# Performance work log

Measured on AMD Instinct MI355X. Metric: run time of the kernel, lower is better.

## Reference

```python
import jax, jax.numpy as jnp
import numpy as np

B, S, D, H = 32, 512, 640, 10
DK = D // H           # 64
NUM_ITER = 3          # capsule routing iterations


def _proj(x, W, b):
    # [B,S,D] @ [D,D]^T -> split heads -> [B,H,S,DK]
    b_, s_, _ = x.shape
    return (x @ W.T + b).reshape(b_, s_, H, DK).transpose(0, 2, 1, 3)


def _squash(t, eps=1e-9):
    sn = jnp.sum(t * t, axis=-1, keepdims=True)
    return (sn / (1.0 + sn)) * t / jnp.sqrt(sn + eps)


def setup_inputs() -> dict:
    key0 = jax.random.key(0)
    ks = jax.random.split(key0, 12)
    s = 1.0 / np.sqrt(D)
    return {
        "query": jax.random.normal(ks[0], (B, S, D), jnp.float32),
        "key": jax.random.normal(ks[1], (B, S, D), jnp.float32),
        "value": jax.random.normal(ks[2], (B, S, D), jnp.float32),
        "mask": jax.random.randint(ks[3], (B, 1, S, S), 0, 2, jnp.int32),
        "adj": jax.random.uniform(ks[4], (B, S, S), jnp.float32),
        "layer": 2,
        "Wq": jax.random.normal(ks[5], (D, D), jnp.float32) * s,
        "bq": jnp.zeros((D,), jnp.float32),
        "Wk": jax.random.normal(ks[6], (D, D), jnp.float32) * s,
        "bk": jnp.zeros((D,), jnp.float32),
        "Wv": jax.random.normal(ks[7], (D, D), jnp.float32) * s,
        "bv": jnp.zeros((D,), jnp.float32),
        # capsule route weights: [num_capsules=1, num_route_nodes=H, DK, D]
        "route_weights": jax.random.normal(ks[8], (1, H, DK, D), jnp.float32) * 0.05,
    }


def reference(query, key, value, mask, adj, layer,
              Wq, bq, Wk, bk, Wv, bv, route_weights):
    q = _proj(query, Wq, bq)   # [B,H,S,DK]
    k = _proj(key, Wk, bk)
    v = _proj(value, Wv, bv)

    # scaled dot-product scores, adjacency + layer-dependent modulation
    scores = jnp.einsum('bhqd,bhkd->bhqk', q, k) / jnp.sqrt(jnp.float32(DK))
    scores = scores + adj[:, None, :, :] / jnp.float32(layer + 1)
    scores = jnp.where(mask == 0, jnp.float32(-1e9), scores)
    p_attn = jax.nn.softmax(scores, axis=-1)            # [B,H,S,S]
    x = jnp.einsum('bhqk,bhkd->bhqd', p_attn, v)        # [B,H,S,DK]

    # [B,H,S,DK] -> [B*S, H, DK]: per-token capsule routing over heads
    x = x.transpose(0, 2, 1, 3).reshape(B * S, H, DK)

    # priors: [num_caps=1, N, H(route nodes), D]
    priors = jnp.einsum('nri,crio->cnro', x, route_weights)
    logits = jnp.zeros(priors.shape[:-1] + (1,), priors.dtype)  # [1,N,H,1]
    out = None
    for i in range(NUM_ITER):
        probs = jax.nn.softmax(logits, axis=2)                  # over route nodes
        out = _squash(jnp.sum(probs * priors, axis=2, keepdims=True))  # [1,N,1,D]
        if i != NUM_ITER - 1:
            logits = logits + jnp.sum(priors * out, axis=-1, keepdims=True)

    return out.reshape(B, S, D)
```

## Files before the change

### kernel.cpp

```cpp
#include <hip/hip_runtime.h>
#include <stdint.h>

#define BB 32
#define SS 512
#define DD 640
#define HH 10
#define DKK 64
#define NTOK (BB*SS)

using f32x4  = __attribute__((ext_vector_type(4))) float;
using bf16x8 = __attribute__((ext_vector_type(8))) __bf16;
using u32x4  = __attribute__((ext_vector_type(4))) unsigned int;
using u32x2  = __attribute__((ext_vector_type(2))) unsigned int;
using u16x4  = __attribute__((ext_vector_type(4))) unsigned short;
using i32x4  = __attribute__((ext_vector_type(4))) int;

__device__ inline unsigned short f2bf(float f){
  union { float f; unsigned int u; } v; v.f=f;
  unsigned int u=v.u;
  u += 0x7FFFu + ((u>>16)&1u);
  return (unsigned short)(u>>16);
}
__device__ inline float bf2f(unsigned short s){
  union { unsigned int u; float f; } v; v.u = ((unsigned int)s)<<16;
  return v.f;
}
__device__ inline unsigned int cvtpk_bf16(float lo, float hi){
  unsigned int r;
  asm volatile("v_cvt_pk_bf16_f32 %0, %1, %2" : "=v"(r) : "v"(lo), "v"(hi));
  return r;
}
__device__ inline void gload_lds16(const unsigned short* g, unsigned short* l){
  __builtin_amdgcn_global_load_lds(
      (const __attribute__((address_space(1))) unsigned int*)g,
      (__attribute__((address_space(3))) unsigned int*)l, 16, 0, 0);
}

__global__ void convert_qkv(const float* __restrict__ q, const float* __restrict__ k,
                            const float* __restrict__ v,
                            unsigned short* __restrict__ xq, unsigned short* __restrict__ xk,
                            unsigned short* __restrict__ xv){
  int i = blockIdx.x*blockDim.x + threadIdx.x;
  const int n4 = (NTOK*DD)/4;
  for (; i < n4; i += gridDim.x*blockDim.x){
    f32x4 a = ((const f32x4*)q)[i];
    f32x4 b = ((const f32x4*)k)[i];
    f32x4 c = ((const f32x4*)v)[i];
    u16x4 ra, rb, rc;
    #pragma unroll
    for (int j=0;j<4;j++){ ra[j]=f2bf(a[j]); rb[j]=f2bf(b[j]); rc[j]=f2bf(c[j]); }
    ((u16x4*)xq)[i]=ra; ((u16x4*)xk)[i]=rb; ((u16x4*)xv)[i]=rc;
  }
}

__global__ void convert_w(const float* __restrict__ wq, const float* __restrict__ wk,
                          const float* __restrict__ wv, const float* __restrict__ rw,
                          unsigned short* __restrict__ bwq, unsigned short* __restrict__ bwk,
                          unsigned short* __restrict__ bwv, unsigned short* __restrict__ brwt){
  int i = blockIdx.x*blockDim.x + threadIdx.x;
  if (i < DD*DD){
    bwq[i]=f2bf(wq[i]); bwk[i]=f2bf(wk[i]); bwv[i]=f2bf(wv[i]);
    unsigned short r = f2bf(rw[i]);
    int ri = i / DD, o = i % DD;
    brwt[o*DD + ri] = r;
  }
}

__global__ void bias_kernel(const int* __restrict__ mask, const float* __restrict__ adj,
                            const int* __restrict__ layer, unsigned short* __restrict__ biasT){
  float sc = 1.0f/(float)(layer[0]+1);
  int i = blockIdx.x*blockDim.x + threadIdx.x;
  const int n4 = (BB*SS*SS)/4;
  for (; i < n4; i += gridDim.x*blockDim.x){
    i32x4 m = ((const i32x4*)mask)[i];
    f32x4 a = ((const f32x4*)adj)[i];
    u16x4 r;
    #pragma unroll
    for (int j=0;j<4;j++) r[j] = m[j] ? f2bf(a[j]*sc) : f2bf(-1e9f);
    const int e  = i*4;
    const int bb = e >> 18;
    const int qq = (e >> 9) & 511;
    const int kk = e & 511;
    const int idx = (((bb*32 + (qq>>4))*32 + (kk>>4))<<8) + ((qq&15)<<4) + (kk&15);
    *(u16x4*)(biasT + idx) = r;
  }
}

#define BM 128
#define BN 128
#define BK 32

template<typename EPI>
__device__ inline void gemm_body(const unsigned short* __restrict__ A,
                                 const unsigned short* __restrict__ W,
                                 int m0, int n0, EPI&& epi)
{
  __shared__ unsigned short As[2][BM*BK];
  __shared__ unsigned short Ws[2][BN*BK];
  const int tid  = threadIdx.x;
  const int lane = tid & 63;
  const int wave = tid >> 6;
  const int wr   = (wave >> 1) * 64;
  const int wc   = (wave & 1) * 64;
  const int l15  = lane & 15;
  const int g    = lane >> 4;

  f32x4 acc[4][4];
  #pragma unroll
  for (int i=0;i<4;i++)
    #pragma unroll
    for (int j=0;j<4;j++){ f32x4 z = {0.f,0.f,0.f,0.f}; acc[i][j]=z; }

  const int srow  = (lane >> 2);
  const int sunit = (lane & 3) ^ ((lane >> 3) & 3);
  const unsigned short* Ag0 = A + (int64_t)(m0 + wave*32 + srow)*DD + sunit*8;
  const unsigned short* Ag1 = A + (int64_t)(m0 + wave*32 + 16 + srow)*DD + sunit*8;
  const unsigned short* Wg0 = W + (int64_t)(n0 + wave*32 + srow)*DD + sunit*8;
  const unsigned short* Wg1 = W + (int64_t)(n0 + wave*32 + 16 + srow)*DD + sunit*8;

  auto stage = [&](int buf, int k0){
    gload_lds16(Ag0 + k0, As[buf] + wave*1024);
    gload_lds16(Ag1 + k0, As[buf] + wave*1024 + 512);
    gload_lds16(Wg0 + k0, Ws[buf] + wave*1024);
    gload_lds16(Wg1 + k0, Ws[buf] + wave*1024 + 512);
  };

  const int fro = (g ^ ((l15 >> 1) & 3)) * 8;

  stage(0, 0);
  int it = 0;
  for (int k0 = 0; k0 < DD; k0 += BK, it++){
    const int buf = it & 1;
    __syncthreads();
    if (k0 + BK < DD) stage(buf^1, k0 + BK);
    bf16x8 af[4], wf[4];
    #pragma unroll
    for (int m=0;m<4;m++) af[m] = *(const bf16x8*)&As[buf][(wr + m*16 + l15)*BK + fro];
    #pragma unroll
    for (int n=0;n<4;n++) wf[n] = *(const bf16x8*)&Ws[buf][(wc + n*16 + l15)*BK + fro];
    #pragma unroll
    for (int m=0;m<4;m++)
      #pragma unroll
      for (int n=0;n<4;n++)
        acc[m][n] = __builtin_amdgcn_mfma_f32_16x16x32_bf16(af[m], wf[n], acc[m][n], 0,0,0);
  }

  #pragma unroll
  for (int m=0;m<4;m++){
    const int rowbase = m0 + wr + m*16 + g*4;
    #pragma unroll
    for (int n=0;n<4;n++){
      const int col = n0 + wc + n*16 + l15;
      #pragma unroll
      for (int r=0;r<4;r++)
        epi(rowbase + r, col, acc[m][n][r]);
    }
  }
}

__global__ __launch_bounds__(256)
void qkv_gemm(const unsigned short* __restrict__ Xq, const unsigned short* __restrict__ Xk,
              const unsigned short* __restrict__ Xv,
              const unsigned short* __restrict__ bWq, const unsigned short* __restrict__ bWk,
              const unsigned short* __restrict__ bWv,
              const float* __restrict__ bq, const float* __restrict__ bk,
              const float* __restrict__ bv,
              unsigned short* __restrict__ qbuf, unsigned short* __restrict__ kbuf,
              unsigned short* __restrict__ vTbuf)
{
  const int y   = blockIdx.y;
  const int sel = y / 5;
  const int n0  = (y % 5) * BN;
  const int m0  = blockIdx.x * BM;
  const unsigned short* A = sel==0 ? Xq  : sel==1 ? Xk  : Xv;
  const unsigned short* W = sel==0 ? bWq : sel==1 ? bWk : bWv;
  const float*          bb= sel==0 ? bq  : sel==1 ? bk  : bv;
  unsigned short* outp    = sel==0 ? qbuf : kbuf;

  gemm_body(A, W, m0, n0, [&](int row, int col, float v){
    float val = v + bb[col];
    int b=row>>9, s=row&511, h=col>>6, dk=col&63;
    if (sel < 2)
      outp[(((int64_t)(b*HH + h))*SS + s)*DKK + dk] = f2bf(val);
    else
      vTbuf[(((int64_t)(b*HH + h))*DKK + dk)*SS + s] = f2bf(val);
  });
}

__global__ __launch_bounds__(256)
void final_gemm(const unsigned short* __restrict__ A, const unsigned short* __restrict__ W,
                float* __restrict__ outp)
{
  gemm_body(A, W, blockIdx.x*BM, blockIdx.y*BN, [&](int row, int col, float v){
    outp[(int64_t)row*DD + col] = v;
  });
}

__global__ __launch_bounds__(256)
void attn_kernel(const unsigned short* __restrict__ qb, const unsigned short* __restrict__ kb,
                 const unsigned short* __restrict__ vT, const unsigned short* __restrict__ biasT,
                 unsigned short* __restrict__ xout)
{
  __shared__ unsigned short SH[20480];
  unsigned short* Kl = SH;
  unsigned short* Vl = SH + 8192;
  char* Pall = (char*)(SH + 16384);

  const int tid  = threadIdx.x;
  const int lane = tid & 63;
  const int wave = tid >> 6;
  const int l15  = lane & 15;
  const int g    = lane >> 4;

  const int orig = blockIdx.x;
  const int wgid = (orig & 7)*320 + (orig >> 3);
  const int h  = wgid % 10;
  const int qt = (wgid / 10) & 7;
  const int b  = wgid / 80;
  const int bh = b*HH + h;

  const unsigned short* Q  = qb + (int64_t)bh*SS*DKK;
  const unsigned short* K  = kb + (int64_t)bh*SS*DKK;
  const unsigned short* V  = vT + (int64_t)bh*DKK*SS;
  const unsigned short* Bt = biasT + (int64_t)((b*32 + qt*4 + wave)*32)*256
                           + l15*16 + g*4;

  const int q0 = qt*64 + wave*16;
  char* Pb = Pall + wave*2048;

  const int srow8 = lane >> 3;
  const int sunit = (lane & 7) ^ (srow8 & 7);

  bf16x8 qf[2];
  #pragma unroll
  for (int ks=0; ks<2; ks++)
    qf[ks] = *(const bf16x8*)(Q + (q0 + l15)*DKK + ks*32 + g*8);

  auto stage = [&](int c, int buf){
    #pragma unroll
    for (int c2=0;c2<2;c2++){
      const int i = wave*2 + c2;
      gload_lds16(K + (int64_t)(c*64 + i*8 + srow8)*DKK + sunit*8,
                  Kl + buf*4096 + i*512);
      gload_lds16(V + (int64_t)(i*8 + srow8)*SS + c*64 + sunit*8,
                  Vl + buf*4096 + i*512);
    }
  };

  float lsum = 0.f;
  f32x4 oacc[4];
  #pragma unroll
  for (int n=0;n<4;n++){ f32x4 z={0.f,0.f,0.f,0.f}; oacc[n]=z; }

  u16x4 bvc[4], bvn[4];
  #pragma unroll
  for (int j=0;j<4;j++) bvc[j] = *(const u16x4*)(Bt + j*256);

  stage(0, 0);
  for (int c = 0; c < 8; c++){
    const int buf = c & 1;
    __syncthreads();
    if (c < 7){
      stage(c+1, buf^1);
      #pragma unroll
      for (int j=0;j<4;j++) bvn[j] = *(const u16x4*)(Bt + ((c+1)*4 + j)*256);
    }

    f32x4 sc[4];
    #pragma unroll
    for (int j=0;j<4;j++){ f32x4 z={0.f,0.f,0.f,0.f}; sc[j]=z; }
    #pragma unroll
    for (int ks=0; ks<2; ks++){
      #pragma unroll
      for (int j=0;j<4;j++){
        bf16x8 kf = *(const bf16x8*)((char*)(Kl + buf*4096)
                     + (j*16 + l15)*128 + (((ks*4+g) ^ (l15&7))*16));
        sc[j] = __builtin_amdgcn_mfma_f32_16x16x32_bf16(kf, qf[ks], sc[j], 0,0,0);
      }
    }
    #pragma unroll
    for (int j=0;j<4;j++){
      float p[4];
      #pragma unroll
      for (int r=0;r<4;r++){
        float s = __builtin_fmaf(sc[j][r], 0.125f, bf2f(bvc[j][r]));
        p[r] = __expf(s - 8.0f);
        lsum += p[r];
      }
      unsigned int w0 = cvtpk_bf16(p[0], p[1]);
      unsigned int w1 = cvtpk_bf16(p[2], p[3]);
      const int kk = j*16 + g*4;
      const int sw = (kk >> 3) ^ (l15 & 7);
      u32x2 w; w[0]=w0; w[1]=w1;
      *(u32x2*)(Pb + l15*128 + sw*16 + (kk&7)*2) = w;
    }
    #pragma unroll
    for (int kt=0; kt<2; kt++){
      bf16x8 pf = *(const bf16x8*)(Pb + l15*128 + (((kt*4+g) ^ (l15&7))*16));
      #pragma unroll
      for (int n=0;n<4;n++){
        bf16x8 vf = *(const bf16x8*)((char*)(Vl + buf*4096)
                     + (n*16 + l15)*128 + (((kt*4+g) ^ (l15&7))*16));
        oacc[n] = __builtin_amdgcn_mfma_f32_16x16x32_bf16(pf, vf, oacc[n], 0,0,0);
      }
    }
    #pragma unroll
    for (int j=0;j<4;j++) bvc[j] = bvn[j];
  }

  lsum += __shfl_xor(lsum, 16);
  lsum += __shfl_xor(lsum, 32);
  const float inv = 1.0f / lsum;
  float invr[4];
  #pragma unroll
  for (int r=0;r<4;r++) invr[r] = __shfl(inv, g*4 + r);

  #pragma unroll
  for (int n=0;n<4;n++){
    const int dk = n*16 + l15;
    #pragma unroll
    for (int r=0;r<4;r++){
      const int qrow = q0 + g*4 + r;
      const int ntok = b*SS + qrow;
      xout[(int64_t)ntok*DD + h*DKK + dk] = f2bf(oacc[n][r] * invr[r]);
    }
  }
}

__global__ __launch_bounds__(256)
void gram_kernel(const unsigned short* __restrict__ x,
                 const unsigned short* __restrict__ RWT,
                 unsigned short* __restrict__ xw)
{
  __shared__ unsigned short Xl[16*664];
  __shared__ float Gp[4][16][56];
  __shared__ float Gfin[16][56];
  __shared__ float Pr[16][10];
  __shared__ float Dm[16][10];
  __shared__ float Lg[16][10];
  __shared__ float wl[16][10];

  const int tid  = threadIdx.x;
  const int lane = tid & 63;
  const int wave = tid >> 6;
  const int l15  = lane & 15;
  const int g    = lane >> 4;
  const int tok0 = blockIdx.x * 16;

  #pragma unroll
  for (int rd=0; rd<5; rd++){
    const int idx = rd*2048 + tid*8;
    const int tk  = idx / 640;
    const int cl  = idx - tk*640;
    u32x4 vv = *(const u32x4*)(x + (int64_t)tok0*640 + idx);
    *(u32x4*)&Xl[tk*664 + cl] = vv;
  }
  __syncthreads();

  float Gacc[55];
  #pragma unroll
  for (int p=0;p<55;p++) Gacc[p]=0.f;

  for (int ot=0; ot<10; ot++){
    const int o0 = (wave*10 + ot)*16;
    f32x4 P[10];
    #pragma unroll
    for (int r=0;r<10;r++){ f32x4 z={0.f,0.f,0.f,0.f}; P[r]=z; }
    #pragma unroll
    for (int r=0;r<10;r++){
      #pragma unroll
      for (int ks=0;ks<2;ks++){
        bf16x8 af = *(const bf16x8*)&RWT[(int64_t)(o0+l15)*DD + r*64 + ks*32 + g*8];
        bf16x8 xf = *(const bf16x8*)&Xl[l15*664 + r*64 + ks*32 + g*8];
        P[r] = __builtin_amdgcn_mfma_f32_16x16x32_bf16(af, xf, P[r], 0,0,0);
      }
    }
    #pragma unroll
    for (int r=0;r<10;r++)
      #pragma unroll
      for (int rp=r; rp<10; rp++){
        const int T = r*10 - r*(r-1)/2 + (rp-r);
        Gacc[T] += P[r][0]*P[rp][0] + P[r][1]*P[rp][1]
                 + P[r][2]*P[rp][2] + P[r][3]*P[rp][3];
      }
  }
  #pragma unroll
  for (int p=0;p<55;p++){
    Gacc[p] += __shfl_xor(Gacc[p], 16);
    Gacc[p] += __shfl_xor(Gacc[p], 32);
  }
  if (lane < 16){
    #pragma unroll
    for (int p=0;p<55;p++) Gp[wave][lane][p] = Gacc[p];
  }
  __syncthreads();
  {
    const int gtok = tid & 15;
    for (int p = tid>>4; p < 55; p += 16)
      Gfin[gtok][p] = Gp[0][gtok][p]+Gp[1][gtok][p]+Gp[2][gtok][p]+Gp[3][gtok][p];
  }
  __syncthreads();

  const int tok = tid >> 4, rp = tid & 15;
  const bool act = rp < 10;
  float grow[10]; float Lr = 0.f;
  if (act){
    #pragma unroll
    for (int r=0;r<10;r++){
      const int lo = r < rp ? r : rp, hi = r < rp ? rp : r;
      grow[r] = Gfin[tok][lo*10 - lo*(lo-1)/2 + (hi-lo)];
    }
    Pr[tok][rp] = 0.1f;
  }
  __syncthreads();
  for (int it=0; it<3; it++){
    float d = 0.f;
    if (act){
      #pragma unroll
      for (int r=0;r<10;r++) d += grow[r]*Pr[tok][r];
      Dm[tok][rp] = d;
    }
    __syncthreads();
    if (act){
      float sn = 0.f;
      #pragma unroll
      for (int r=0;r<10;r++) sn += Dm[tok][r]*Pr[tok][r];
      const float sc = (sn/(1.f+sn))*rsqrtf(sn+1e-9f);
      if (it < 2){ Lr += sc*d; Lg[tok][rp] = Lr; }
      else        wl[tok][rp] = sc*Pr[tok][rp];
    }
    __syncthreads();
    if (it < 2){
      if (act){
        float mx = Lg[tok][0];
        #pragma unroll
        for (int r=1;r<10;r++) mx = fmaxf(mx, Lg[tok][r]);
        float se = 0.f;
        #pragma unroll
        for (int r=0;r<10;r++) se += __expf(Lg[tok][r]-mx);
        Pr[tok][rp] = __expf(Lr-mx)/se;
      }
      __syncthreads();
    }
  }

  {
    const int tk = tid >> 4, seg = tid & 15;
    #pragma unroll
    for (int j=0;j<5;j++){
      const int c = seg*40 + j*8;
      const float w = wl[tk][c>>6];
      u16x4 a = *(const u16x4*)&Xl[tk*664 + c];
      u16x4 b = *(const u16x4*)&Xl[tk*664 + c + 4];
      u32x4 o;
      o[0] = cvtpk_bf16(bf2f(a[0])*w, bf2f(a[1])*w);
      o[1] = cvtpk_bf16(bf2f(a[2])*w, bf2f(a[3])*w);
      o[2] = cvtpk_bf16(bf2f(b[0])*w, bf2f(b[1])*w);
      o[3] = cvtpk_bf16(bf2f(b[2])*w, bf2f(b[3])*w);
      *(u32x4*)&xw[(int64_t)(tok0+tk)*DD + c] = o;
    }
  }
}

extern "C" void kernel_launch(void* const* d_in, const int* in_sizes, int n_in,
                              void* d_out, int out_size, void* d_ws, size_t ws_size,
                              hipStream_t stream)
{
  (void)in_sizes; (void)n_in; (void)out_size; (void)ws_size;
  const float* q    = (const float*)d_in[0];
  const float* k    = (const float*)d_in[1];
  const float* v    = (const float*)d_in[2];
  const int*   mask = (const int*)d_in[3];
  const float* adj  = (const float*)d_in[4];
  const int*   layer= (const int*)d_in[5];
  const float* Wq   = (const float*)d_in[6];
  const float* bq   = (const float*)d_in[7];
  const float* Wk   = (const float*)d_in[8];
  const float* bk   = (const float*)d_in[9];
  const float* Wv   = (const float*)d_in[10];
  const float* bv   = (const float*)d_in[11];
  const float* rw   = (const float*)d_in[12];

  char* ws = (char*)d_ws;
  size_t off = 0;
  auto alloc = [&](size_t sz)->char*{ char* p = ws + off; off += (sz + 255) & ~(size_t)255; return p; };
  const size_t SZX = (size_t)NTOK*DD*2;
  unsigned short* Xq    = (unsigned short*)alloc(SZX);
  unsigned short* Xk    = (unsigned short*)alloc(SZX);
  unsigned short* Xv    = (unsigned short*)alloc(SZX);
  unsigned short* bWq   = (unsigned short*)alloc((size_t)DD*DD*2);
  unsigned short* bWk   = (unsigned short*)alloc((size_t)DD*DD*2);
  unsigned short* bWv   = (unsigned short*)alloc((size_t)DD*DD*2);
  unsigned short* bRWT  = (unsigned short*)alloc((size_t)DD*DD*2);
  unsigned short* qbuf  = (unsigned short*)alloc(SZX);
  unsigned short* kbuf  = (unsigned short*)alloc(SZX);
  unsigned short* vTbuf = (unsigned short*)alloc(SZX);
  unsigned short* biasb = (unsigned short*)alloc((size_t)BB*SS*SS*2);
  unsigned short* xout  = Xq;
  unsigned short* xw    = Xk;

  convert_qkv<<<2048,256,0,stream>>>(q,k,v,Xq,Xk,Xv);
  convert_w<<<1600,256,0,stream>>>(Wq,Wk,Wv,rw,bWq,bWk,bWv,bRWT);
  bias_kernel<<<2048,256,0,stream>>>(mask,adj,layer,biasb);

  dim3 gq(NTOK/BM, 15);
  qkv_gemm<<<gq,256,0,stream>>>(Xq,Xk,Xv,bWq,bWk,bWv,bq,bk,bv,qbuf,kbuf,vTbuf);

  attn_kernel<<<2560,256,0,stream>>>(qbuf,kbuf,vTbuf,biasb,xout);

  gram_kernel<<<NTOK/16,256,0,stream>>>(xout,bRWT,xw);

  dim3 gf(NTOK/BM, DD/BN);
  final_gemm<<<gf,256,0,stream>>>(xw,bRWT,(float*)d_out);
}
```

Before: 325.1 us.

## Split gram kernel over output chunks and pre-swizzle route weights

Result: faster. 298.5 us (-8.2%).

```diff
diff --git a/kernel.cpp b/kernel.cpp
--- a/kernel.cpp
+++ b/kernel.cpp
@@ -56,13 +56,19 @@
 __global__ void convert_w(const float* __restrict__ wq, const float* __restrict__ wk,
                           const float* __restrict__ wv, const float* __restrict__ rw,
                           unsigned short* __restrict__ bwq, unsigned short* __restrict__ bwk,
-                          unsigned short* __restrict__ bwv, unsigned short* __restrict__ brwt){
+                          unsigned short* __restrict__ bwv, unsigned short* __restrict__ brwt,
+                          unsigned short* __restrict__ brwtf){
   int i = blockIdx.x*blockDim.x + threadIdx.x;
   if (i < DD*DD){
     bwq[i]=f2bf(wq[i]); bwk[i]=f2bf(wk[i]); bwv[i]=f2bf(wv[i]);
-    unsigned short r = f2bf(rw[i]);
-    int ri = i / DD, o = i % DD;
-    brwt[o*DD + ri] = r;
+    unsigned short rv = f2bf(rw[i]);
+    const int kk = i / DD;
+    const int o  = i % DD;
+    brwt[o*DD + kk] = rv;
+    const int r  = kk >> 6, ii = kk & 63;
+    const int ks = ii >> 5, rem = ii & 31, g = rem >> 3, j = rem & 7;
+    const int oT = o >> 4, l15o = o & 15;
+    brwtf[(size_t)((oT*10 + r)*2 + ks)*512 + (g*16 + l15o)*8 + j] = rv;
   }
 }
 
@@ -328,17 +334,12 @@
 }
 
 __global__ __launch_bounds__(256)
-void gram_kernel(const unsigned short* __restrict__ x,
-                 const unsigned short* __restrict__ RWT,
-                 unsigned short* __restrict__ xw)
+void gram_part(const unsigned short* __restrict__ x,
+               const unsigned short* __restrict__ RWTf,
+               float* __restrict__ Gpart)
 {
   __shared__ unsigned short Xl[16*664];
-  __shared__ float Gp[4][16][56];
-  __shared__ float Gfin[16][56];
-  __shared__ float Pr[16][10];
-  __shared__ float Dm[16][10];
-  __shared__ float Lg[16][10];
-  __shared__ float wl[16][10];
+  __shared__ float Gp[4][16][57];
 
   const int tid  = threadIdx.x;
   const int lane = tid & 63;
@@ -346,6 +347,7 @@
   const int l15  = lane & 15;
   const int g    = lane >> 4;
   const int tok0 = blockIdx.x * 16;
+  const int oc   = blockIdx.y;
 
   #pragma unroll
   for (int rd=0; rd<5; rd++){
@@ -361,8 +363,10 @@
   #pragma unroll
   for (int p=0;p<55;p++) Gacc[p]=0.f;
 
-  for (int ot=0; ot<10; ot++){
-    const int o0 = (wave*10 + ot)*16;
+  #pragma unroll
+  for (int ot2=0; ot2<2; ot2++){
+    const int oTile = oc*8 + wave*2 + ot2;
+    const unsigned short* base = RWTf + (size_t)oTile*10240;
     f32x4 P[10];
     #pragma unroll
     for (int r=0;r<10;r++){ f32x4 z={0.f,0.f,0.f,0.f}; P[r]=z; }
@@ -370,7 +374,7 @@
     for (int r=0;r<10;r++){
       #pragma unroll
       for (int ks=0;ks<2;ks++){
-        bf16x8 af = *(const bf16x8*)&RWT[(int64_t)(o0+l15)*DD + r*64 + ks*32 + g*8];
+        bf16x8 af = *(const bf16x8*)&base[(r*2+ks)*512 + lane*8];
         bf16x8 xf = *(const bf16x8*)&Xl[l15*664 + r*64 + ks*32 + g*8];
         P[r] = __builtin_amdgcn_mfma_f32_16x16x32_bf16(af, xf, P[r], 0,0,0);
       }
@@ -397,7 +401,33 @@
   {
     const int gtok = tid & 15;
     for (int p = tid>>4; p < 55; p += 16)
-      Gfin[gtok][p] = Gp[0][gtok][p]+Gp[1][gtok][p]+Gp[2][gtok][p]+Gp[3][gtok][p];
+      Gpart[((size_t)oc*NTOK + tok0 + gtok)*56 + p]
+        = Gp[0][gtok][p]+Gp[1][gtok][p]+Gp[2][gtok][p]+Gp[3][gtok][p];
+  }
+}
+
+__global__ __launch_bounds__(256)
+void route_xw(const float* __restrict__ Gpart, const unsigned short* __restrict__ x,
+              unsigned short* __restrict__ xw)
+{
+  __shared__ float Gfin[16][57];
+  __shared__ float Pr[16][10];
+  __shared__ float Dm[16][10];
+  __shared__ float Lg[16][10];
+  __shared__ float wl[16][10];
+
+  const int tid  = threadIdx.x;
+  const int tok0 = blockIdx.x * 16;
+
+  {
+    const int gtok = tid & 15;
+    for (int p = tid>>4; p < 55; p += 16){
+      float s = 0.f;
+      #pragma unroll
+      for (int oc=0; oc<5; oc++)
+        s += Gpart[((size_t)oc*NTOK + tok0 + gtok)*56 + p];
+      Gfin[gtok][p] = s;
+    }
   }
   __syncthreads();
 
@@ -444,21 +474,20 @@
     }
   }
 
-  {
-    const int tk = tid >> 4, seg = tid & 15;
-    #pragma unroll
-    for (int j=0;j<5;j++){
-      const int c = seg*40 + j*8;
-      const float w = wl[tk][c>>6];
-      u16x4 a = *(const u16x4*)&Xl[tk*664 + c];
-      u16x4 b = *(const u16x4*)&Xl[tk*664 + c + 4];
-      u32x4 o;
-      o[0] = cvtpk_bf16(bf2f(a[0])*w, bf2f(a[1])*w);
-      o[1] = cvtpk_bf16(bf2f(a[2])*w, bf2f(a[3])*w);
-      o[2] = cvtpk_bf16(bf2f(b[0])*w, bf2f(b[1])*w);
-      o[3] = cvtpk_bf16(bf2f(b[2])*w, bf2f(b[3])*w);
-      *(u32x4*)&xw[(int64_t)(tok0+tk)*DD + c] = o;
-    }
+  #pragma unroll
+  for (int e=0; e<5; e++){
+    const int idx = e*2048 + tid*8;
+    const int tk  = idx / 640;
+    const int cl  = idx - tk*640;
+    const float w = wl[tk][cl>>6];
+    u16x4 a = *(const u16x4*)(x + (int64_t)tok0*640 + idx);
+    u16x4 b = *(const u16x4*)(x + (int64_t)tok0*640 + idx + 4);
+    u32x4 o;
+    o[0] = cvtpk_bf16(bf2f(a[0])*w, bf2f(a[1])*w);
+    o[1] = cvtpk_bf16(bf2f(a[2])*w, bf2f(a[3])*w);
+    o[2] = cvtpk_bf16(bf2f(b[0])*w, bf2f(b[1])*w);
+    o[3] = cvtpk_bf16(bf2f(b[2])*w, bf2f(b[3])*w);
+    *(u32x4*)&xw[(int64_t)tok0*640 + idx] = o;
   }
 }
 
@@ -492,15 +521,17 @@
   unsigned short* bWk   = (unsigned short*)alloc((size_t)DD*DD*2);
   unsigned short* bWv   = (unsigned short*)alloc((size_t)DD*DD*2);
   unsigned short* bRWT  = (unsigned short*)alloc((size_t)DD*DD*2);
+  unsigned short* bRWTf = (unsigned short*)alloc((size_t)DD*DD*2);
   unsigned short* qbuf  = (unsigned short*)alloc(SZX);
   unsigned short* kbuf  = (unsigned short*)alloc(SZX);
   unsigned short* vTbuf = (unsigned short*)alloc(SZX);
   unsigned short* biasb = (unsigned short*)alloc((size_t)BB*SS*SS*2);
+  float*          Gpart = (float*)alloc((size_t)5*NTOK*56*4);
   unsigned short* xout  = Xq;
   unsigned short* xw    = Xk;
 
   convert_qkv<<<2048,256,0,stream>>>(q,k,v,Xq,Xk,Xv);
-  convert_w<<<1600,256,0,stream>>>(Wq,Wk,Wv,rw,bWq,bWk,bWv,bRWT);
+  convert_w<<<1600,256,0,stream>>>(Wq,Wk,Wv,rw,bWq,bWk,bWv,bRWT,bRWTf);
   bias_kernel<<<2048,256,0,stream>>>(mask,adj,layer,biasb);
 
   dim3 gq(NTOK/BM, 15);
@@ -508,7 +539,9 @@
 
   attn_kernel<<<2560,256,0,stream>>>(qbuf,kbuf,vTbuf,biasb,xout);
 
-  gram_kernel<<<NTOK/16,256,0,stream>>>(xout,bRWT,xw);
+  dim3 gp(NTOK/16, 5);
+  gram_part<<<gp,256,0,stream>>>(xout,bRWTf,Gpart);
+  route_xw<<<NTOK/16,256,0,stream>>>(Gpart,xout,xw);
 
   dim3 gf(NTOK/BM, DD/BN);
   final_gemm<<<gf,256,0,stream>>>(xw,bRWT,(float*)d_out);
```
